# Performance work log

Hardware: AMD Instinct MI355X
Metric: run time of the kernel (lower is better)

## Reference

```python
import jax, jax.numpy as jnp
import numpy as np

B, T, D = 2, 2048, 1024
F = 4096
E = 8


def setup_inputs() -> dict:
    key = jax.random.key(0)
    k0, k1, k2, k3 = jax.random.split(key, 4)
    x = jax.random.normal(k0, (B, T, D), dtype=jnp.float32)
    Wg = jax.random.normal(k1, (E, D), dtype=jnp.float32) * 0.02   # gate Linear weight [E, D]
    W1 = jax.random.normal(k2, (E, D, F), dtype=jnp.float32) * 0.02  # expert up-proj
    W2 = jax.random.normal(k3, (E, F, D), dtype=jnp.float32) * 0.02  # expert down-proj
    return {"x": x, "Wg": Wg, "W1": W1, "W2": W2}


def reference(x, Wg, W1, W2):
    b, t, d = x.shape
    h = x.reshape(-1, d)                              # [N, D], N = b*t
    # --- top-2 gate ---
    logits = h @ Wg.T                                 # [N, E]
    scores, idx = jax.lax.top_k(logits, 2)            # [N, 2], [N, 2]
    scores = jax.nn.softmax(scores.astype(jnp.float32), axis=-1).astype(x.dtype)
    # --- all-expert dense FFN (SiLU MLP) ---
    up = jnp.einsum('nd,edf->enf', h, W1)             # [E, N, F]
    act = jax.nn.silu(up)
    out = jnp.einsum('enf,efd->ned', act, W2)         # [N, E, D]
    # --- combine top-2 ---
    sel = jnp.take_along_axis(out, idx[:, :, None], axis=1)  # [N, 2, D]
    y = jnp.sum(scores[:, :, None] * sel, axis=1)     # [N, D]
    return y.reshape(b, t, d)
```

## Files before the change

kernel.cpp:

```cpp
#include <hip/hip_runtime.h>
#include <hip/hip_bf16.h>
#include <stdint.h>

#define N_TOK 4096
#define D_DIM 1024
#define F_DIM 4096
#define E_NUM 8

typedef unsigned short u16;
typedef __attribute__((ext_vector_type(8))) short short8;
typedef __attribute__((ext_vector_type(4))) float f32x4;

__device__ __forceinline__ u16 f2bf(float f) {
  union { float f; uint32_t u; } v; v.f = f;
  uint32_t u = v.u;
  uint32_t r = (u + 0x7FFFu + ((u >> 16) & 1u)) >> 16;
  return (u16)r;
}

__device__ __forceinline__ void gld_lds16(const u16* g, u16* l) {
  __builtin_amdgcn_global_load_lds(
      (const __attribute__((address_space(1))) uint32_t*)g,
      (__attribute__((address_space(3))) uint32_t*)l, 16, 0, 0);
}

__global__ __launch_bounds__(256) void transpose_cvt_kernel(
    const float* __restrict__ in, u16* __restrict__ out, int R, int C) {
  __shared__ u16 tile[64][72];
  int e = blockIdx.z;
  int r0 = blockIdx.y * 64, c0 = blockIdx.x * 64;
  const float* src = in + (size_t)e * R * C;
  u16* dst = out + (size_t)e * R * C;
  int tid = threadIdx.x;
  int lr = tid & 15;
  int rr = tid >> 4;
#pragma unroll
  for (int p = 0; p < 4; ++p) {
    int r = rr + p * 16;
    float4 v = *(const float4*)&src[(size_t)(r0 + r) * C + c0 + lr * 4];
    tile[lr * 4 + 0][r] = f2bf(v.x);
    tile[lr * 4 + 1][r] = f2bf(v.y);
    tile[lr * 4 + 2][r] = f2bf(v.z);
    tile[lr * 4 + 3][r] = f2bf(v.w);
  }
  __syncthreads();
#pragma unroll
  for (int p = 0; p < 4; ++p) {
    int c = rr + p * 16;
    ushort4 o = *(const ushort4*)&tile[c][lr * 4];
    *(ushort4*)&dst[(size_t)(c0 + c) * R + r0 + lr * 4] = o;
  }
}

__global__ void gate_kernel(const float* __restrict__ x, const float* __restrict__ Wg,
                            u16* __restrict__ xb, int2* __restrict__ choice,
                            float* __restrict__ sc2) {
  int n = blockIdx.x;
  int l = threadIdx.x;
  const float* xr = x + (size_t)n * D_DIM;
  u16* xbr = xb + (size_t)n * D_DIM;
  float acc[E_NUM];
#pragma unroll
  for (int e = 0; e < E_NUM; ++e) acc[e] = 0.f;
  for (int d = l; d < D_DIM; d += 64) {
    float xv = xr[d];
    xbr[d] = f2bf(xv);
#pragma unroll
    for (int e = 0; e < E_NUM; ++e) acc[e] += xv * Wg[e * D_DIM + d];
  }
#pragma unroll
  for (int e = 0; e < E_NUM; ++e) {
    float v = acc[e];
#pragma unroll
    for (int off = 32; off > 0; off >>= 1) v += __shfl_xor(v, off);
    acc[e] = v;
  }
  if (l == 0) {
    int i0 = 0; float m0 = acc[0];
#pragma unroll
    for (int e = 1; e < E_NUM; ++e) if (acc[e] > m0) { m0 = acc[e]; i0 = e; }
    int i1 = -1; float m1 = -INFINITY;
#pragma unroll
    for (int e = 0; e < E_NUM; ++e) if (e != i0 && acc[e] > m1) { m1 = acc[e]; i1 = e; }
    float z = expf(m1 - m0);
    float s0 = 1.f / (1.f + z);
    sc2[n * 2 + 0] = s0;
    sc2[n * 2 + 1] = 1.f - s0;
    choice[n] = make_int2(i0, i1);
  }
}

__global__ void route_kernel(const int2* __restrict__ choice, int* __restrict__ cnt,
                             int* __restrict__ tok_list) {
  int e = blockIdx.x;
  int l = threadIdx.x;
  unsigned long long below = (l == 0) ? 0ull : ((~0ull) >> (64 - l));
  int c = 0;
  for (int it = 0; it < N_TOK / 64; ++it) {
    int n = it * 64 + l;
    int2 ch = choice[n];
    unsigned long long b0 = __ballot(ch.x == e);
    if (ch.x == e) tok_list[e * N_TOK + c + __popcll(b0 & below)] = 2 * n;
    c += __popcll(b0);
    unsigned long long b1 = __ballot(ch.y == e);
    if (ch.y == e) tok_list[e * N_TOK + c + __popcll(b1 & below)] = 2 * n + 1;
    c += __popcll(b1);
  }
  if (l == 0) cnt[e] = c;
}

__global__ void prefix_kernel(const int* __restrict__ cnt, int* __restrict__ base) {
  if (threadIdx.x == 0) {
    int s = 0;
    for (int e = 0; e < E_NUM; ++e) { base[e] = s; s += cnt[e]; }
  }
}


__global__ __launch_bounds__(256) void up_gemm(
    const u16* __restrict__ xb, const u16* __restrict__ w1t,
    const int* __restrict__ cnt, const int* __restrict__ base,
    const int* __restrict__ tok_list, u16* __restrict__ act) {
  __shared__ u16 As[128 * 32];
  __shared__ u16 Bs[128 * 32];

  const int bid = blockIdx.x;
  const int orig = (bid & 7) * 1024 + (bid >> 3);
  const int bx = orig & 31, by = (orig >> 5) & 31, e = orig >> 10;

  const int ce = cnt[e];
  const int row0 = by * 128;
  if (row0 >= ce) return;
  const int col0 = bx * 128;
  const int be = base[e];

  const int tid = threadIdx.x;
  const int wave = tid >> 6, lane = tid & 63;
  const int wm = wave >> 1, wn = wave & 1;
  const int lr = lane & 15, kq = lane >> 4;

  const int rs0 = wave * 32 + (lane >> 2);
  const int rs1 = rs0 + 16;
  const int kb = (((lane & 3) ^ ((lane >> 3) & 3)) * 8);
  const int kq8 = ((kq ^ ((lr >> 1) & 3)) * 8);

  int ga0 = row0 + rs0, ga1 = row0 + rs1;
  int e0 = (ga0 < ce) ? (tok_list[e * N_TOK + ga0] & (2 * N_TOK - 1)) : 0;
  int e1 = (ga1 < ce) ? (tok_list[e * N_TOK + ga1] & (2 * N_TOK - 1)) : 0;
  const u16* srcA0 = xb + (e0 >> 1) * D_DIM + kb;
  const u16* srcA1 = xb + (e1 >> 1) * D_DIM + kb;
  const u16* srcB0 = w1t + (size_t)(e * F_DIM + col0 + rs0) * D_DIM + kb;
  const u16* srcB1 = w1t + (size_t)(e * F_DIM + col0 + rs1) * D_DIM + kb;
  u16* ldsA0 = As + (wave * 2 + 0) * 512;
  u16* ldsA1 = As + (wave * 2 + 1) * 512;
  u16* ldsB0 = Bs + (wave * 2 + 0) * 512;
  u16* ldsB1 = Bs + (wave * 2 + 1) * 512;

  f32x4 acc[4][4];
#pragma unroll
  for (int m = 0; m < 4; ++m)
#pragma unroll
    for (int n = 0; n < 4; ++n) acc[m][n] = (f32x4){0.f, 0.f, 0.f, 0.f};

  for (int k0 = 0; k0 < D_DIM; k0 += 32) {
    gld_lds16(srcA0 + k0, ldsA0);
    gld_lds16(srcA1 + k0, ldsA1);
    gld_lds16(srcB0 + k0, ldsB0);
    gld_lds16(srcB1 + k0, ldsB1);
    __syncthreads();
    short8 a[4], b[4];
#pragma unroll
    for (int m = 0; m < 4; ++m)
      a[m] = *(const short8*)&As[(wm * 64 + m * 16 + lr) * 32 + kq8];
#pragma unroll
    for (int n = 0; n < 4; ++n)
      b[n] = *(const short8*)&Bs[(wn * 64 + n * 16 + lr) * 32 + kq8];
#pragma unroll
    for (int m = 0; m < 4; ++m)
#pragma unroll
      for (int n = 0; n < 4; ++n)
        acc[m][n] = __builtin_amdgcn_mfma_f32_16x16x32_bf16(a[m], b[n], acc[m][n], 0, 0, 0);
    __syncthreads();
  }

#pragma unroll
  for (int m = 0; m < 4; ++m) {
#pragma unroll
    for (int rg = 0; rg < 4; ++rg) {
      int row = wm * 64 + m * 16 + kq * 4 + rg;
      int i = row0 + row;
      if (i < ce) {
        u16* dst = act + (size_t)(be + i) * F_DIM + col0 + wn * 64;
#pragma unroll
        for (int n = 0; n < 4; ++n) {
          float v = acc[m][n][rg];
          float s = v / (1.f + expf(-v));
          dst[n * 16 + lr] = f2bf(s);
        }
      }
    }
  }
}

__global__ __launch_bounds__(512) void down_gemm(
    const u16* __restrict__ act, const u16* __restrict__ w2t,
    const int* __restrict__ cnt, const int* __restrict__ base,
    const int* __restrict__ tok_list, const float* __restrict__ sc2,
    float* __restrict__ out) {
  __shared__ u16 As[128 * 32];
  __shared__ u16 Bs[128 * 32];
  __shared__ int toks[128];

  const int bid = blockIdx.x;
  const int orig = (bid & 7) * 256 + (bid >> 3);
  const int bx = orig & 7, by = (orig >> 3) & 31, e = orig >> 8;

  const int ce = cnt[e];
  const int row0 = by * 128;
  if (row0 >= ce) return;
  const int col0 = bx * 128;
  const int be = base[e];

  const int tid = threadIdx.x;
  const int wave = tid >> 6, lane = tid & 63;
  const int wm = wave >> 2, wn = wave & 3;
  const int lr = lane & 15, kq = lane >> 4;

  if (tid < 128) {
    int i = row0 + tid;
    toks[tid] = (i < ce) ? tok_list[e * N_TOK + i] : -1;
  }

  const int rsA = wave * 16 + (lane >> 2);
  const int kb = (((lane & 3) ^ ((lane >> 3) & 3)) * 8);
  const int kq8 = ((kq ^ ((lr >> 1) & 3)) * 8);

  int ra = min(be + row0 + rsA, 2 * N_TOK - 1);
  const u16* srcA = act + (size_t)ra * F_DIM + kb;
  const u16* srcB = w2t + (size_t)(e * D_DIM + col0 + rsA) * F_DIM + kb;
  u16* ldsA = As + wave * 512;
  u16* ldsB = Bs + wave * 512;

  f32x4 acc[4][2];
#pragma unroll
  for (int m = 0; m < 4; ++m)
#pragma unroll
    for (int n = 0; n < 2; ++n) acc[m][n] = (f32x4){0.f, 0.f, 0.f, 0.f};

  for (int k0 = 0; k0 < F_DIM; k0 += 32) {
    gld_lds16(srcA + k0, ldsA);
    gld_lds16(srcB + k0, ldsB);
    __syncthreads();
    short8 a[4], b[2];
#pragma unroll
    for (int m = 0; m < 4; ++m)
      a[m] = *(const short8*)&As[(wm * 64 + m * 16 + lr) * 32 + kq8];
#pragma unroll
    for (int n = 0; n < 2; ++n)
      b[n] = *(const short8*)&Bs[(wn * 32 + n * 16 + lr) * 32 + kq8];
#pragma unroll
    for (int m = 0; m < 4; ++m)
#pragma unroll
      for (int n = 0; n < 2; ++n)
        acc[m][n] = __builtin_amdgcn_mfma_f32_16x16x32_bf16(a[m], b[n], acc[m][n], 0, 0, 0);
    __syncthreads();
  }

#pragma unroll
  for (int m = 0; m < 4; ++m) {
#pragma unroll
    for (int rg = 0; rg < 4; ++rg) {
      int row = wm * 64 + m * 16 + kq * 4 + rg;
      int ent = toks[row];
      if (ent >= 0) {
        int tokn = ent >> 1;
        float sc = sc2[tokn * 2 + (ent & 1)];
        float* dst = out + (size_t)tokn * D_DIM + col0 + wn * 32;
#pragma unroll
        for (int n = 0; n < 2; ++n)
          atomicAdd(&dst[n * 16 + lr], acc[m][n][rg] * sc);
      }
    }
  }
}

extern "C" void kernel_launch(void* const* d_in, const int* in_sizes, int n_in,
                              void* d_out, int out_size, void* d_ws, size_t ws_size,
                              hipStream_t stream) {
  const float* x  = (const float*)d_in[0];
  const float* Wg = (const float*)d_in[1];
  const float* W1 = (const float*)d_in[2];
  const float* W2 = (const float*)d_in[3];
  float* out = (float*)d_out;

  char* ws = (char*)d_ws;
  size_t off = 0;
  u16* xb  = (u16*)(ws + off); off += (size_t)N_TOK * D_DIM * 2;
  u16* w1t = (u16*)(ws + off); off += (size_t)E_NUM * F_DIM * D_DIM * 2;
  u16* w2t = (u16*)(ws + off); off += (size_t)E_NUM * D_DIM * F_DIM * 2;
  u16* act = (u16*)(ws + off); off += (size_t)2 * N_TOK * F_DIM * 2;
  int* tok_list = (int*)(ws + off); off += (size_t)E_NUM * N_TOK * 4;
  float* sc2 = (float*)(ws + off); off += (size_t)N_TOK * 2 * 4;
  int2* choice = (int2*)(ws + off); off += (size_t)N_TOK * 8;
  int* cnt  = (int*)(ws + off); off += 128;
  int* base = (int*)(ws + off); off += 128;

  hipMemsetAsync(d_out, 0, (size_t)out_size * 4, stream);

  {
    dim3 blk(256, 1, 1);
    dim3 g1(F_DIM / 64, D_DIM / 64, E_NUM);
    transpose_cvt_kernel<<<g1, blk, 0, stream>>>(W1, w1t, D_DIM, F_DIM);
    dim3 g2(D_DIM / 64, F_DIM / 64, E_NUM);
    transpose_cvt_kernel<<<g2, blk, 0, stream>>>(W2, w2t, F_DIM, D_DIM);
  }

  gate_kernel<<<N_TOK, 64, 0, stream>>>(x, Wg, xb, choice, sc2);
  route_kernel<<<E_NUM, 64, 0, stream>>>(choice, cnt, tok_list);
  prefix_kernel<<<1, 1, 0, stream>>>(cnt, base);

  up_gemm<<<dim3(8192), 256, 0, stream>>>(xb, w1t, cnt, base, tok_list, act);
  down_gemm<<<dim3(2048), 512, 0, stream>>>(act, w2t, cnt, base, tok_list, sc2, out);
}
```

Before: 336.9 us.

## Double-buffer LDS in down_gemm with async prefetch and use fast exp

The down-projection GEMM now keeps two LDS stages, loading tile t+2 while computing on tile t. Explicit vmcnt waits and barriers replace the single-buffer load/sync/compute pattern, so global-to-LDS latency can overlap with MFMA work. It also swaps expf for __expf in the gate softmax and the SiLU, which slightly reduces accuracy. The manual waitcnt scheme is fragile if the compiler inserts extra memory operations.

```diff
diff --git a/kernel.cpp b/kernel.cpp
--- a/kernel.cpp
+++ b/kernel.cpp
@@ -82,7 +82,7 @@
     int i1 = -1; float m1 = -INFINITY;
 #pragma unroll
     for (int e = 0; e < E_NUM; ++e) if (e != i0 && acc[e] > m1) { m1 = acc[e]; i1 = e; }
-    float z = expf(m1 - m0);
+    float z = __expf(m1 - m0);
     float s0 = 1.f / (1.f + z);
     sc2[n * 2 + 0] = s0;
     sc2[n * 2 + 1] = 1.f - s0;
@@ -194,7 +194,7 @@
 #pragma unroll
         for (int n = 0; n < 4; ++n) {
           float v = acc[m][n][rg];
-          float s = v / (1.f + expf(-v));
+          float s = v / (1.f + __expf(-v));
           dst[n * 16 + lr] = f2bf(s);
         }
       }
@@ -207,8 +207,8 @@
     const int* __restrict__ cnt, const int* __restrict__ base,
     const int* __restrict__ tok_list, const float* __restrict__ sc2,
     float* __restrict__ out) {
-  __shared__ u16 As[128 * 32];
-  __shared__ u16 Bs[128 * 32];
+  __shared__ u16 As[2][128 * 32];
+  __shared__ u16 Bs[2][128 * 32];
   __shared__ int toks[128];
 
   const int bid = blockIdx.x;
@@ -230,6 +230,7 @@
     int i = row0 + tid;
     toks[tid] = (i < ce) ? tok_list[e * N_TOK + i] : -1;
   }
+  __syncthreads();
 
   const int rsA = wave * 16 + (lane >> 2);
   const int kb = (((lane & 3) ^ ((lane >> 3) & 3)) * 8);
@@ -238,8 +239,6 @@
   int ra = min(be + row0 + rsA, 2 * N_TOK - 1);
   const u16* srcA = act + (size_t)ra * F_DIM + kb;
   const u16* srcB = w2t + (size_t)(e * D_DIM + col0 + rsA) * F_DIM + kb;
-  u16* ldsA = As + wave * 512;
-  u16* ldsB = Bs + wave * 512;
 
   f32x4 acc[4][2];
 #pragma unroll
@@ -247,24 +246,48 @@
 #pragma unroll
     for (int n = 0; n < 2; ++n) acc[m][n] = (f32x4){0.f, 0.f, 0.f, 0.f};
 
-  for (int k0 = 0; k0 < F_DIM; k0 += 32) {
-    gld_lds16(srcA + k0, ldsA);
-    gld_lds16(srcB + k0, ldsB);
-    __syncthreads();
-    short8 a[4], b[2];
-#pragma unroll
-    for (int m = 0; m < 4; ++m)
-      a[m] = *(const short8*)&As[(wm * 64 + m * 16 + lr) * 32 + kq8];
-#pragma unroll
-    for (int n = 0; n < 2; ++n)
-      b[n] = *(const short8*)&Bs[(wn * 32 + n * 16 + lr) * 32 + kq8];
-#pragma unroll
-    for (int m = 0; m < 4; ++m)
-#pragma unroll
-      for (int n = 0; n < 2; ++n)
-        acc[m][n] = __builtin_amdgcn_mfma_f32_16x16x32_bf16(a[m], b[n], acc[m][n], 0, 0, 0);
-    __syncthreads();
-  }
+#define DSTAGE(k0, b)                              \
+  do {                                             \
+    gld_lds16(srcA + (k0), &As[b][wave * 512]);    \
+    gld_lds16(srcB + (k0), &Bs[b][wave * 512]);    \
+  } while (0)
+
+#define DCOMPUTE(b)                                                           \
+  do {                                                                        \
+    short8 a[4], bb[2];                                                       \
+    _Pragma("unroll") for (int m = 0; m < 4; ++m)                             \
+        a[m] = *(const short8*)&As[b][(wm * 64 + m * 16 + lr) * 32 + kq8];    \
+    _Pragma("unroll") for (int n = 0; n < 2; ++n)                             \
+        bb[n] = *(const short8*)&Bs[b][(wn * 32 + n * 16 + lr) * 32 + kq8];   \
+    _Pragma("unroll") for (int m = 0; m < 4; ++m)                             \
+        _Pragma("unroll") for (int n = 0; n < 2; ++n)                         \
+            acc[m][n] = __builtin_amdgcn_mfma_f32_16x16x32_bf16(a[m], bb[n], acc[m][n], 0, 0, 0); \
+  } while (0)
+
+  const int NT = F_DIM / 32;
+  DSTAGE(0, 0);
+  DSTAGE(32, 1);
+  asm volatile("s_waitcnt vmcnt(2)" ::: "memory");
+  __builtin_amdgcn_s_barrier();
+  __builtin_amdgcn_sched_barrier(0);
+  int cur = 0;
+  for (int t = 0; t < NT; ++t) {
+    DCOMPUTE(cur);
+    __builtin_amdgcn_sched_barrier(0);
+    __builtin_amdgcn_s_barrier();
+    __builtin_amdgcn_sched_barrier(0);
+    if (t + 2 < NT) {
+      DSTAGE((t + 2) * 32, cur);
+      asm volatile("s_waitcnt vmcnt(2)" ::: "memory");
+    } else {
+      asm volatile("s_waitcnt vmcnt(0)" ::: "memory");
+    }
+    __builtin_amdgcn_s_barrier();
+    __builtin_amdgcn_sched_barrier(0);
+    cur ^= 1;
+  }
+#undef DSTAGE
+#undef DCOMPUTE
 
 #pragma unroll
   for (int m = 0; m < 4; ++m) {
```

New measurement: 327.2 us. -2.9%, faster.
